# Performance work log

Measured on AMD Instinct MI355X. Metric: run time of the kernel, lower is better.

## Reference

```python
import jax, jax.numpy as jnp
import numpy as np

D_MODEL = 1024
D_HIDDEN = 32   # per-head MPS bond dimension
N_HEADS = 8
D_FF = 4096
EPS_LN = 1e-5
EPS_NORM = 1e-6


def layernorm(x, g, b):
    m = jnp.mean(x, axis=-1, keepdims=True)
    v = jnp.mean(jnp.square(x - m), axis=-1, keepdims=True)
    return (x - m) * jax.lax.rsqrt(v + EPS_LN) * g + b


def mps_recurrence(x, Wa, ba, h0, Wo, bo):
    # x: [B,S,D]. Per-token per-head transfer matrices A_t in R^{dh x dh}.
    B, S, D = x.shape
    A = (x @ Wa + ba).reshape(B, S, N_HEADS, D_HIDDEN, D_HIDDEN)
    A = jnp.moveaxis(A, 1, 0)  # [S,B,H,dh,dh]
    h_init = jnp.broadcast_to(h0, (B, N_HEADS, D_HIDDEN))  # [B,H,dh]

    def step(h, A_t):
        h = jnp.einsum('bhij,bhj->bhi', A_t, h)
        h = h / (jnp.linalg.norm(h, axis=-1, keepdims=True) + EPS_NORM)
        return h, h

    _, ys = jax.lax.scan(step, h_init, A)          # ys: [S,B,H,dh]
    ys = jnp.moveaxis(ys, 0, 1).reshape(B, S, N_HEADS * D_HIDDEN)
    return ys @ Wo + bo                            # [B,S,D]


def setup_inputs() -> dict:
    key = jax.random.key(0)
    ks = jax.random.split(key, 12)
    B, S, D = 4, 2048, D_MODEL
    inv = 1.0 / np.sqrt(D)
    inv_hd = 1.0 / np.sqrt(N_HEADS * D_HIDDEN)
    return {
        'x': jax.random.normal(ks[0], (B, S, D), jnp.float32),
        'ln1_g': jnp.ones((D,), jnp.float32),
        'ln1_b': jnp.zeros((D,), jnp.float32),
        'Wa': jax.random.normal(ks[1], (D, N_HEADS * D_HIDDEN * D_HIDDEN), jnp.float32) * inv,
        'ba': jnp.zeros((N_HEADS * D_HIDDEN * D_HIDDEN,), jnp.float32),
        'h0': jax.random.normal(ks[2], (N_HEADS, D_HIDDEN), jnp.float32) / np.sqrt(D_HIDDEN),
        'Wo': jax.random.normal(ks[3], (N_HEADS * D_HIDDEN, D), jnp.float32) * inv_hd,
        'bo': jnp.zeros((D,), jnp.float32),
        'ln2_g': jnp.ones((D,), jnp.float32),
        'ln2_b': jnp.zeros((D,), jnp.float32),
        'W1': jax.random.normal(ks[4], (D, D_FF), jnp.float32) * inv,
        'b1': jnp.zeros((D_FF,), jnp.float32),
        'W2': jax.random.normal(ks[5], (D_FF, D), jnp.float32) / np.sqrt(D_FF),
        'b2': jnp.zeros((D,), jnp.float32),
    }


def reference(x, ln1_g, ln1_b, Wa, ba, h0, Wo, bo, ln2_g, ln2_b, W1, b1, W2, b2):
    # Dropout in eval mode (identity).
    x = x + mps_recurrence(layernorm(x, ln1_g, ln1_b), Wa, ba, h0, Wo, bo)
    h = layernorm(x, ln2_g, ln2_b)
    ffn = jax.nn.gelu(h @ W1 + b1, approximate=False) @ W2 + b2
    return x + ffn
```

## Files before the change

kernel.cpp:

```cpp
#include <hip/hip_runtime.h>
#include <hip/hip_bf16.h>
#include <math.h>

typedef float f32x4 __attribute__((ext_vector_type(4)));
typedef __bf16 bf16x4 __attribute__((ext_vector_type(4)));
typedef __bf16 bf16x8 __attribute__((ext_vector_type(8)));

#define AS1(p) ((const __attribute__((address_space(1))) void*)(p))
#define AS3(p) ((__attribute__((address_space(3))) void*)(p))

static constexpr int D_MODEL = 1024;
static constexpr int S_LEN   = 2048;
static constexpr int BATCH   = 4;
static constexpr int NTOK    = BATCH * S_LEN;
static constexpr int NH      = 8;
static constexpr int DH      = 32;
static constexpr int NA      = NH * DH * DH;
static constexpr int D_FF    = 4096;
static constexpr int CHUNK   = 16;
static constexpr int NCHUNK  = S_LEN / CHUNK;

__global__ __launch_bounds__(256) void transpose_bf16(
    const float* __restrict__ in, __bf16* __restrict__ out, int R, int C) {
  __shared__ float tile[32][33];
  int tx = threadIdx.x & 31, ty = threadIdx.x >> 5;
  int c0 = blockIdx.x * 32, r0 = blockIdx.y * 32;
  for (int i = ty; i < 32; i += 8)
    tile[i][tx] = in[(size_t)(r0 + i) * C + c0 + tx];
  __syncthreads();
  for (int i = ty; i < 32; i += 8)
    out[(size_t)(c0 + i) * R + r0 + tx] = (__bf16)tile[tx][i];
}

__global__ __launch_bounds__(256) void transpose_split(
    const float* __restrict__ in, __bf16* __restrict__ ohi,
    __bf16* __restrict__ olo, int R, int C) {
  __shared__ float tile[32][33];
  int tx = threadIdx.x & 31, ty = threadIdx.x >> 5;
  int c0 = blockIdx.x * 32, r0 = blockIdx.y * 32;
  for (int i = ty; i < 32; i += 8)
    tile[i][tx] = in[(size_t)(r0 + i) * C + c0 + tx];
  __syncthreads();
  for (int i = ty; i < 32; i += 8) {
    float v = tile[tx][i];
    __bf16 h = (__bf16)v;
    ohi[(size_t)(c0 + i) * R + r0 + tx] = h;
    olo[(size_t)(c0 + i) * R + r0 + tx] = (__bf16)(v - (float)h);
  }
}

template <int MODE>
__global__ __launch_bounds__(256) void ln_kernel(
    const float* __restrict__ in, const float* __restrict__ g,
    const float* __restrict__ bta, void* __restrict__ outv,
    void* __restrict__ outv2) {
  int row = blockIdx.x, tid = threadIdx.x;
  const float4* in4 = (const float4*)(in + (size_t)row * D_MODEL);
  float4 v = in4[tid];
  float s  = v.x + v.y + v.z + v.w;
  float ss = v.x * v.x + v.y * v.y + v.z * v.z + v.w * v.w;
  for (int o = 32; o; o >>= 1) { s += __shfl_down(s, o); ss += __shfl_down(ss, o); }
  __shared__ float ps[4], pq[4];
  int lane = tid & 63, w = tid >> 6;
  if (lane == 0) { ps[w] = s; pq[w] = ss; }
  __syncthreads();
  s  = ps[0] + ps[1] + ps[2] + ps[3];
  ss = pq[0] + pq[1] + pq[2] + pq[3];
  float mean = s * (1.0f / D_MODEL);
  float var  = ss * (1.0f / D_MODEL) - mean * mean;
  float inv  = rsqrtf(fmaxf(var, 0.0f) + 1e-5f);
  float4 gv = ((const float4*)g)[tid];
  float4 bv = ((const float4*)bta)[tid];
  float o0 = (v.x - mean) * inv * gv.x + bv.x;
  float o1 = (v.y - mean) * inv * gv.y + bv.y;
  float o2 = (v.z - mean) * inv * gv.z + bv.z;
  float o3 = (v.w - mean) * inv * gv.w + bv.w;
  if (MODE == 1) {
    float4 o = {o0, o1, o2, o3};
    ((float4*)outv)[(size_t)row * (D_MODEL / 4) + tid] = o;
  } else if (MODE == 0) {
    bf16x4 o;
    o[0] = (__bf16)o0; o[1] = (__bf16)o1; o[2] = (__bf16)o2; o[3] = (__bf16)o3;
    ((bf16x4*)outv)[(size_t)row * (D_MODEL / 4) + tid] = o;
  } else {
    bf16x4 oh, ol;
    oh[0] = (__bf16)o0; oh[1] = (__bf16)o1; oh[2] = (__bf16)o2; oh[3] = (__bf16)o3;
    ol[0] = (__bf16)(o0 - (float)oh[0]);
    ol[1] = (__bf16)(o1 - (float)oh[1]);
    ol[2] = (__bf16)(o2 - (float)oh[2]);
    ol[3] = (__bf16)(o3 - (float)oh[3]);
    ((bf16x4*)outv )[(size_t)row * (D_MODEL / 4) + tid] = oh;
    ((bf16x4*)outv2)[(size_t)row * (D_MODEL / 4) + tid] = ol;
  }
}

__global__ __launch_bounds__(256) void gemm_split_f32out(
    const __bf16* __restrict__ Ahi, const __bf16* __restrict__ Alo,
    const __bf16* __restrict__ BThi, const __bf16* __restrict__ BTlo,
    const float* __restrict__ bias, float* __restrict__ out,
    int M, int N, int K) {
  __shared__ __bf16 Ash[128 * 32], Asl[128 * 32];
  __shared__ __bf16 Bsh[128 * 32], Bsl[128 * 32];
  const int tid = threadIdx.x;
  const int lane = tid & 63, w = tid >> 6;
  const int m0 = blockIdx.y * 128, n0 = blockIdx.x * 128;
  const int wm = (w >> 1) * 64, wn = (w & 1) * 64;

  f32x4 acc[4][4];
#pragma unroll
  for (int a = 0; a < 4; a++)
#pragma unroll
    for (int b = 0; b < 4; b++)
#pragma unroll
      for (int r = 0; r < 4; r++) acc[a][b][r] = 0.0f;

  const int srow = tid >> 2;
  const int soff = (tid & 3) * 16;
  const size_t goff0 = (size_t)(m0 + srow) * K + (soff >> 1);
  const size_t goff1 = (size_t)(m0 + srow + 64) * K + (soff >> 1);
  const size_t hoff0 = (size_t)(n0 + srow) * K + (soff >> 1);
  const size_t hoff1 = (size_t)(n0 + srow + 64) * K + (soff >> 1);
  const int l0 = srow * 64 + soff, l1 = (srow + 64) * 64 + soff;

  const int fm = lane & 15, fq = lane >> 4;
  for (int k0 = 0; k0 < K; k0 += 32) {
    __builtin_amdgcn_global_load_lds(AS1(Ahi + goff0 + k0), AS3((char*)Ash + l0), 16, 0, 0);
    __builtin_amdgcn_global_load_lds(AS1(Ahi + goff1 + k0), AS3((char*)Ash + l1), 16, 0, 0);
    __builtin_amdgcn_global_load_lds(AS1(Alo + goff0 + k0), AS3((char*)Asl + l0), 16, 0, 0);
    __builtin_amdgcn_global_load_lds(AS1(Alo + goff1 + k0), AS3((char*)Asl + l1), 16, 0, 0);
    __builtin_amdgcn_global_load_lds(AS1(BThi + hoff0 + k0), AS3((char*)Bsh + l0), 16, 0, 0);
    __builtin_amdgcn_global_load_lds(AS1(BThi + hoff1 + k0), AS3((char*)Bsh + l1), 16, 0, 0);
    __builtin_amdgcn_global_load_lds(AS1(BTlo + hoff0 + k0), AS3((char*)Bsl + l0), 16, 0, 0);
    __builtin_amdgcn_global_load_lds(AS1(BTlo + hoff1 + k0), AS3((char*)Bsl + l1), 16, 0, 0);
    __syncthreads();
    bf16x8 ah[4], al[4], bh[4], bl[4];
#pragma unroll
    for (int t = 0; t < 4; t++) {
      int o = (wm + t * 16 + fm) * 64 + fq * 16;
      ah[t] = *(const bf16x8*)((const char*)Ash + o);
      al[t] = *(const bf16x8*)((const char*)Asl + o);
    }
#pragma unroll
    for (int t = 0; t < 4; t++) {
      int o = (wn + t * 16 + fm) * 64 + fq * 16;
      bh[t] = *(const bf16x8*)((const char*)Bsh + o);
      bl[t] = *(const bf16x8*)((const char*)Bsl + o);
    }
#pragma unroll
    for (int tm = 0; tm < 4; tm++)
#pragma unroll
      for (int tn = 0; tn < 4; tn++) {
        acc[tm][tn] = __builtin_amdgcn_mfma_f32_16x16x32_bf16(ah[tm], bh[tn], acc[tm][tn], 0, 0, 0);
        acc[tm][tn] = __builtin_amdgcn_mfma_f32_16x16x32_bf16(ah[tm], bl[tn], acc[tm][tn], 0, 0, 0);
        acc[tm][tn] = __builtin_amdgcn_mfma_f32_16x16x32_bf16(al[tm], bh[tn], acc[tm][tn], 0, 0, 0);
      }
    __syncthreads();
  }

#pragma unroll
  for (int tn = 0; tn < 4; tn++) {
    int col = n0 + wn + tn * 16 + fm;
    float bv = bias[col];
#pragma unroll
    for (int tm = 0; tm < 4; tm++) {
#pragma unroll
      for (int r = 0; r < 4; r++) {
        int row = m0 + wm + tm * 16 + fq * 4 + r;
        out[(size_t)row * N + col] = acc[tm][tn][r] + bv;
      }
    }
  }
}

enum { EPI_BF16_BIAS = 0, EPI_BF16_BIAS_GELU = 1, EPI_F32_BIAS_RES = 2 };

template <int EPI>
__global__ __launch_bounds__(256) void gemm_bf16(
    const __bf16* __restrict__ Amat, const __bf16* __restrict__ BT,
    const float* __restrict__ bias, const float* __restrict__ res,
    void* __restrict__ out, int M, int N, int K) {
  __shared__ __bf16 As[128 * 32];
  __shared__ __bf16 Bs[128 * 32];
  const int tid = threadIdx.x;
  const int lane = tid & 63, w = tid >> 6;
  const int m0 = blockIdx.y * 128, n0 = blockIdx.x * 128;
  const int wm = (w >> 1) * 64, wn = (w & 1) * 64;

  f32x4 acc[4][4];
#pragma unroll
  for (int a = 0; a < 4; a++)
#pragma unroll
    for (int b = 0; b < 4; b++)
#pragma unroll
      for (int r = 0; r < 4; r++) acc[a][b][r] = 0.0f;

  const int srow = tid >> 2;
  const int soff = (tid & 3) * 16;
  const __bf16* gA0 = Amat + (size_t)(m0 + srow) * K + (soff >> 1);
  const __bf16* gA1 = Amat + (size_t)(m0 + srow + 64) * K + (soff >> 1);
  const __bf16* gB0 = BT + (size_t)(n0 + srow) * K + (soff >> 1);
  const __bf16* gB1 = BT + (size_t)(n0 + srow + 64) * K + (soff >> 1);
  char* lA0 = (char*)As + srow * 64 + soff;
  char* lA1 = (char*)As + (srow + 64) * 64 + soff;
  char* lB0 = (char*)Bs + srow * 64 + soff;
  char* lB1 = (char*)Bs + (srow + 64) * 64 + soff;

  const int fm = lane & 15, fq = lane >> 4;
  for (int k0 = 0; k0 < K; k0 += 32) {
    __builtin_amdgcn_global_load_lds(AS1(gA0 + k0), AS3(lA0), 16, 0, 0);
    __builtin_amdgcn_global_load_lds(AS1(gA1 + k0), AS3(lA1), 16, 0, 0);
    __builtin_amdgcn_global_load_lds(AS1(gB0 + k0), AS3(lB0), 16, 0, 0);
    __builtin_amdgcn_global_load_lds(AS1(gB1 + k0), AS3(lB1), 16, 0, 0);
    __syncthreads();
    bf16x8 af[4], bf[4];
#pragma unroll
    for (int t = 0; t < 4; t++)
      af[t] = *(const bf16x8*)((const char*)As + (wm + t * 16 + fm) * 64 + fq * 16);
#pragma unroll
    for (int t = 0; t < 4; t++)
      bf[t] = *(const bf16x8*)((const char*)Bs + (wn + t * 16 + fm) * 64 + fq * 16);
#pragma unroll
    for (int tm = 0; tm < 4; tm++)
#pragma unroll
      for (int tn = 0; tn < 4; tn++)
        acc[tm][tn] = __builtin_amdgcn_mfma_f32_16x16x32_bf16(af[tm], bf[tn], acc[tm][tn], 0, 0, 0);
    __syncthreads();
  }

#pragma unroll
  for (int tn = 0; tn < 4; tn++) {
    int col = n0 + wn + tn * 16 + fm;
    float bv = bias[col];
#pragma unroll
    for (int tm = 0; tm < 4; tm++) {
#pragma unroll
      for (int r = 0; r < 4; r++) {
        int row = m0 + wm + tm * 16 + fq * 4 + r;
        float v = acc[tm][tn][r] + bv;
        size_t idx = (size_t)row * N + col;
        if (EPI == EPI_F32_BIAS_RES) {
          ((float*)out)[idx] = v + res[idx];
        } else if (EPI == EPI_BF16_BIAS_GELU) {
          v = 0.5f * v * (1.0f + erff(v * 0.70710678118654752f));
          ((__bf16*)out)[idx] = (__bf16)v;
        } else {
          ((__bf16*)out)[idx] = (__bf16)v;
        }
      }
    }
  }
}

__global__ __launch_bounds__(64) void mps_chunkprod_f32(
    const float* __restrict__ A, float* __restrict__ P) {
  int bid = blockIdx.x;
  int c = bid & 127, hh = bid >> 7;
  int lane = threadIdx.x;
  int jj = lane & 31, half = lane >> 5;
  __shared__ float Albuf[2][DH * DH];

  float curc[32];
#pragma unroll
  for (int k = 0; k < 32; k++) curc[k] = (k == jj) ? 1.0f : 0.0f;

  const float* Abase = A + (size_t)(c * CHUNK) * NA + (size_t)hh * (DH * DH);

  {
    const float4* src = (const float4*)Abase;
    float4* dst = (float4*)Albuf[0];
#pragma unroll
    for (int r = 0; r < 4; r++) dst[lane + 64 * r] = src[lane + 64 * r];
  }
  __syncthreads();

  for (int t = 0; t < CHUNK; t++) {
    int cb = t & 1;
    float4 pf[4];
    if (t + 1 < CHUNK) {
      const float4* srcn = (const float4*)(Abase + (size_t)(t + 1) * NA);
#pragma unroll
      for (int r = 0; r < 4; r++) pf[r] = srcn[lane + 64 * r];
    }
    float nxt[16];
#pragma unroll
    for (int i16 = 0; i16 < 16; i16++) {
      const float4* ap = (const float4*)&Albuf[cb][(half * 16 + i16) * 32];
      float a0 = 0.f, a1 = 0.f, a2 = 0.f, a3 = 0.f;
#pragma unroll
      for (int k4 = 0; k4 < 8; k4++) {
        float4 av = ap[k4];
        a0 += av.x * curc[k4 * 4 + 0];
        a1 += av.y * curc[k4 * 4 + 1];
        a2 += av.z * curc[k4 * 4 + 2];
        a3 += av.w * curc[k4 * 4 + 3];
      }
      nxt[i16] = (a0 + a1) + (a2 + a3);
    }
#pragma unroll
    for (int i16 = 0; i16 < 16; i16++) {
      float mine  = nxt[i16];
      float other = __shfl_xor(mine, 32);
      curc[i16]      = (half == 0) ? mine  : other;
      curc[16 + i16] = (half == 0) ? other : mine;
    }
    if (t + 1 < CHUNK) {
      float4* dst = (float4*)Albuf[cb ^ 1];
#pragma unroll
      for (int r = 0; r < 4; r++) dst[lane + 64 * r] = pf[r];
      __syncthreads();
    }
  }

  float* Pc = P + (size_t)bid * (DH * DH);
#pragma unroll
  for (int k16 = 0; k16 < 16; k16++) {
    float v = (half == 0) ? curc[k16] : curc[16 + k16];
    Pc[(half * 16 + k16) * 32 + jj] = v;
  }
}

__global__ __launch_bounds__(64) void mps_chunkscan(
    const float* __restrict__ P, const float* __restrict__ h0,
    float* __restrict__ hstart) {
  int hh = blockIdx.x;
  int lane = threadIdx.x, i = lane & 31, half = lane >> 5;
  float hv = h0[hh * 32 + i];
  const float* row = P + (size_t)hh * NCHUNK * (DH * DH) + i * 32 + half * 16;
  int kb = half * 16;

  float4 pf0[4], pf1[4];
#pragma unroll
  for (int r = 0; r < 4; r++) pf0[r] = ((const float4*)row)[r];
#pragma unroll
  for (int r = 0; r < 4; r++) pf1[r] = ((const float4*)(row + DH * DH))[r];

  for (int c = 0; c < NCHUNK; c++) {
    if (lane < 32) hstart[((size_t)hh * NCHUNK + c) * 32 + i] = hv;
    float4 cur[4];
#pragma unroll
    for (int r = 0; r < 4; r++) cur[r] = pf0[r];
#pragma unroll
    for (int r = 0; r < 4; r++) pf0[r] = pf1[r];
    int cn = (c + 2 < NCHUNK) ? (c + 2) : (NCHUNK - 1);
#pragma unroll
    for (int r = 0; r < 4; r++)
      pf1[r] = ((const float4*)(row + (size_t)cn * (DH * DH)))[r];

    float a0 = 0.f, a1 = 0.f, a2 = 0.f, a3 = 0.f;
#pragma unroll
    for (int j4 = 0; j4 < 4; j4++) {
      float4 pv = cur[j4];
      a0 += pv.x * __shfl(hv, kb + j4 * 4 + 0);
      a1 += pv.y * __shfl(hv, kb + j4 * 4 + 1);
      a2 += pv.z * __shfl(hv, kb + j4 * 4 + 2);
      a3 += pv.w * __shfl(hv, kb + j4 * 4 + 3);
    }
    float y = (a0 + a1) + (a2 + a3);
    y += __shfl_xor(y, 32);
    float nn = y * y;
#pragma unroll
    for (int o = 16; o; o >>= 1) nn += __shfl_xor(nn, o);
    hv = y / (sqrtf(nn) + 1e-6f);
  }
}

__global__ __launch_bounds__(64) void mps_expand_f32(
    const float* __restrict__ A, const float* __restrict__ hstart,
    __bf16* __restrict__ ys, int tok0base) {
  int bid = blockIdx.x;
  int c = bid & 127, hh = bid >> 7;
  int lane = threadIdx.x, i = lane & 31, half = lane >> 5;
  float hv = hstart[(size_t)bid * 32 + i];
  const float* Ar = A + (size_t)(c * CHUNK) * NA + (size_t)hh * (DH * DH)
                    + i * 32 + half * 16;
  int kb = half * 16;

  float4 pf[4];
#pragma unroll
  for (int r = 0; r < 4; r++) pf[r] = ((const float4*)Ar)[r];

  for (int t = 0; t < CHUNK; t++) {
    float4 cur[4];
#pragma unroll
    for (int r = 0; r < 4; r++) cur[r] = pf[r];
    if (t + 1 < CHUNK) {
      const float4* an = (const float4*)(Ar + (size_t)(t + 1) * NA);
#pragma unroll
      for (int r = 0; r < 4; r++) pf[r] = an[r];
    }
    float a0 = 0.f, a1 = 0.f, a2 = 0.f, a3 = 0.f;
#pragma unroll
    for (int j4 = 0; j4 < 4; j4++) {
      float4 av = cur[j4];
      a0 += av.x * __shfl(hv, kb + j4 * 4 + 0);
      a1 += av.y * __shfl(hv, kb + j4 * 4 + 1);
      a2 += av.z * __shfl(hv, kb + j4 * 4 + 2);
      a3 += av.w * __shfl(hv, kb + j4 * 4 + 3);
    }
    float y = (a0 + a1) + (a2 + a3);
    y += __shfl_xor(y, 32);
    float nn = y * y;
#pragma unroll
    for (int o = 16; o; o >>= 1) nn += __shfl_xor(nn, o);
    hv = y / (sqrtf(nn) + 1e-6f);
    if (lane < 32)
      ys[(size_t)(tok0base + c * CHUNK + t) * (NH * DH) + hh * 32 + i] = (__bf16)hv;
  }
}

extern "C" void kernel_launch(void* const* d_in, const int* in_sizes, int n_in,
                              void* d_out, int out_size, void* d_ws, size_t ws_size,
                              hipStream_t stream) {
  const float* x     = (const float*)d_in[0];
  const float* ln1_g = (const float*)d_in[1];
  const float* ln1_b = (const float*)d_in[2];
  const float* Wa    = (const float*)d_in[3];
  const float* ba    = (const float*)d_in[4];
  const float* h0    = (const float*)d_in[5];
  const float* Wo    = (const float*)d_in[6];
  const float* bo    = (const float*)d_in[7];
  const float* ln2_g = (const float*)d_in[8];
  const float* ln2_b = (const float*)d_in[9];
  const float* W1    = (const float*)d_in[10];
  const float* b1    = (const float*)d_in[11];
  const float* W2    = (const float*)d_in[12];
  const float* b2    = (const float*)d_in[13];
  float* out = (float*)d_out;

  char* wsb = (char*)d_ws;
  size_t off = 0;
  auto alloc = [&](size_t bytes) -> void* {
    void* p = wsb + off;
    off += (bytes + 255) & ~(size_t)255;
    return p;
  };
  __bf16* WoT   = (__bf16*)alloc((size_t)(NH * DH) * D_MODEL * 2);
  __bf16* W1T   = (__bf16*)alloc((size_t)D_MODEL * D_FF * 2);
  __bf16* W2T   = (__bf16*)alloc((size_t)D_FF * D_MODEL * 2);
  __bf16* ys    = (__bf16*)alloc((size_t)NTOK * NH * DH * 2);
  float*  hst   = (float*) alloc((size_t)NH * NCHUNK * DH * 4);
  __bf16* xnh   = (__bf16*)alloc((size_t)NTOK * D_MODEL * 2);
  __bf16* xnl   = (__bf16*)alloc((size_t)NTOK * D_MODEL * 2);
  __bf16* WaTh  = (__bf16*)alloc((size_t)D_MODEL * NA * 2);
  __bf16* WaTl  = (__bf16*)alloc((size_t)D_MODEL * NA * 2);
  size_t tail0 = off;
  float*  Af32 = (float*) alloc((size_t)S_LEN * NA * 4);
  float*  P    = (float*) alloc((size_t)NH * NCHUNK * DH * DH * 4);
  __bf16* mid  = (__bf16*)(wsb + tail0);

  transpose_bf16<<<dim3(D_MODEL / 32, (NH * DH) / 32), 256, 0, stream>>>(Wo, WoT, NH * DH, D_MODEL);
  transpose_bf16<<<dim3(D_FF / 32, D_MODEL / 32), 256, 0, stream>>>(W1, W1T, D_MODEL, D_FF);
  transpose_bf16<<<dim3(D_MODEL / 32, D_FF / 32), 256, 0, stream>>>(W2, W2T, D_FF, D_MODEL);
  transpose_split<<<dim3(NA / 32, D_MODEL / 32), 256, 0, stream>>>(Wa, WaTh, WaTl, D_MODEL, NA);

  ln_kernel<2><<<NTOK, 256, 0, stream>>>(x, ln1_g, ln1_b, xnh, xnl);

  for (int b = 0; b < BATCH; b++) {
    gemm_split_f32out<<<dim3(NA / 128, S_LEN / 128), 256, 0, stream>>>(
        xnh + (size_t)b * S_LEN * D_MODEL, xnl + (size_t)b * S_LEN * D_MODEL,
        WaTh, WaTl, ba, Af32, S_LEN, NA, D_MODEL);
    mps_chunkprod_f32<<<NH * NCHUNK, 64, 0, stream>>>(Af32, P);
    mps_chunkscan<<<NH, 64, 0, stream>>>(P, h0, hst);
    mps_expand_f32<<<NH * NCHUNK, 64, 0, stream>>>(Af32, hst, ys, b * S_LEN);
  }

  gemm_bf16<EPI_F32_BIAS_RES><<<dim3(D_MODEL / 128, NTOK / 128), 256, 0, stream>>>(
      ys, WoT, bo, x, out, NTOK, D_MODEL, NH * DH);

  ln_kernel<0><<<NTOK, 256, 0, stream>>>(out, ln2_g, ln2_b, xnh, nullptr);

  gemm_bf16<EPI_BF16_BIAS_GELU><<<dim3(D_FF / 128, NTOK / 128), 256, 0, stream>>>(
      xnh, W1T, b1, nullptr, mid, NTOK, D_FF, D_MODEL);

  gemm_bf16<EPI_F32_BIAS_RES><<<dim3(D_MODEL / 128, NTOK / 128), 256, 0, stream>>>(
      mid, W2T, b2, out, out, NTOK, D_MODEL, D_FF);
}
```

Baseline: 1.571 ms.

## Swizzle GEMM blocks across XCDs, fast GELU, LDS-staged vectorized epilogue stores

Adds an XCD-aware block index remap to both GEMM kernels so that consecutive tiles share the L2 of the same die. It replaces erff in the GELU epilogue with an Abramowitz-Stegun polynomial that uses the hardware rcp and exp2 instructions. The GELU epilogue now stages its bf16 results through LDS per wave so each lane writes 16-byte rows instead of scattered 2-byte stores. The risks are slight GELU accuracy loss and the remap assuming the block count divides by 8.

```diff
diff --git a/kernel.cpp b/kernel.cpp
--- a/kernel.cpp
+++ b/kernel.cpp
@@ -19,6 +19,26 @@
 static constexpr int D_FF    = 4096;
 static constexpr int CHUNK   = 16;
 static constexpr int NCHUNK  = S_LEN / CHUNK;
+
+__device__ __forceinline__ void xcd_swizzle(int& bx, int& by) {
+  int gx = gridDim.x;
+  int nwg = gx * gridDim.y;
+  int bid = by * gx + bx;
+  int swz = (bid & 7) * (nwg >> 3) + (bid >> 3);
+  bx = swz % gx;
+  by = swz / gx;
+}
+
+__device__ __forceinline__ float gelu_erf_fast(float v) {
+  float z = fabsf(v) * 0.70710678118654752f;
+  float t = __builtin_amdgcn_rcpf(fmaf(0.3275911f, z, 1.0f));
+  float p = t * (0.254829592f + t * (-0.284496736f + t * (1.421413741f +
+            t * (-1.453152027f + t * 1.061405429f))));
+  float e = __builtin_amdgcn_exp2f(-1.4426950408889634f * z * z);
+  float er = 1.0f - p * e;
+  er = (v < 0.0f) ? -er : er;
+  return 0.5f * v * (1.0f + er);
+}
 
 __global__ __launch_bounds__(256) void transpose_bf16(
     const float* __restrict__ in, __bf16* __restrict__ out, int R, int C) {
@@ -103,7 +123,9 @@
   __shared__ __bf16 Bsh[128 * 32], Bsl[128 * 32];
   const int tid = threadIdx.x;
   const int lane = tid & 63, w = tid >> 6;
-  const int m0 = blockIdx.y * 128, n0 = blockIdx.x * 128;
+  int bx = blockIdx.x, by = blockIdx.y;
+  xcd_swizzle(bx, by);
+  const int m0 = by * 128, n0 = bx * 128;
   const int wm = (w >> 1) * 64, wn = (w & 1) * 64;
 
   f32x4 acc[4][4];
@@ -179,11 +201,14 @@
     const __bf16* __restrict__ Amat, const __bf16* __restrict__ BT,
     const float* __restrict__ bias, const float* __restrict__ res,
     void* __restrict__ out, int M, int N, int K) {
-  __shared__ __bf16 As[128 * 32];
-  __shared__ __bf16 Bs[128 * 32];
+  __shared__ __bf16 smem[2 * 128 * 32];
+  __bf16* As = smem;
+  __bf16* Bs = smem + 128 * 32;
   const int tid = threadIdx.x;
   const int lane = tid & 63, w = tid >> 6;
-  const int m0 = blockIdx.y * 128, n0 = blockIdx.x * 128;
+  int bx = blockIdx.x, by = blockIdx.y;
+  xcd_swizzle(bx, by);
+  const int m0 = by * 128, n0 = bx * 128;
   const int wm = (w >> 1) * 64, wn = (w & 1) * 64;
 
   f32x4 acc[4][4];
@@ -227,24 +252,52 @@
     __syncthreads();
   }
 
-#pragma unroll
-  for (int tn = 0; tn < 4; tn++) {
-    int col = n0 + wn + tn * 16 + fm;
-    float bv = bias[col];
-#pragma unroll
-    for (int tm = 0; tm < 4; tm++) {
-#pragma unroll
-      for (int r = 0; r < 4; r++) {
-        int row = m0 + wm + tm * 16 + fq * 4 + r;
-        float v = acc[tm][tn][r] + bv;
-        size_t idx = (size_t)row * N + col;
-        if (EPI == EPI_F32_BIAS_RES) {
-          ((float*)out)[idx] = v + res[idx];
-        } else if (EPI == EPI_BF16_BIAS_GELU) {
-          v = 0.5f * v * (1.0f + erff(v * 0.70710678118654752f));
-          ((__bf16*)out)[idx] = (__bf16)v;
-        } else {
-          ((__bf16*)out)[idx] = (__bf16)v;
+  if (EPI == EPI_BF16_BIAS_GELU) {
+    float bvs[4];
+#pragma unroll
+    for (int tn = 0; tn < 4; tn++) bvs[tn] = bias[n0 + wn + tn * 16 + fm];
+    char* patch = (char*)smem + w * 4096;
+#pragma unroll
+    for (int h2 = 0; h2 < 2; h2++) {
+#pragma unroll
+      for (int tmi = 0; tmi < 2; tmi++) {
+        int tm = h2 * 2 + tmi;
+#pragma unroll
+        for (int tn = 0; tn < 4; tn++)
+#pragma unroll
+          for (int r = 0; r < 4; r++) {
+            float vv = gelu_erf_fast(acc[tm][tn][r] + bvs[tn]);
+            *(__bf16*)(patch + (tmi * 16 + fq * 4 + r) * 128 + (tn * 16 + fm) * 2) =
+                (__bf16)vv;
+          }
+      }
+      asm volatile("s_waitcnt lgkmcnt(0)" ::: "memory");
+      int lrow = lane >> 3, lcb = (lane & 7) * 16;
+#pragma unroll
+      for (int rr = 0; rr < 4; rr++) {
+        bf16x8 ov = *(const bf16x8*)(patch + (rr * 8 + lrow) * 128 + lcb);
+        size_t grow = (size_t)(m0 + wm + h2 * 32 + rr * 8 + lrow);
+        *(bf16x8*)((__bf16*)out + grow * N + n0 + wn + (lane & 7) * 8) = ov;
+      }
+      if (h2 == 0) asm volatile("s_waitcnt lgkmcnt(0)" ::: "memory");
+    }
+  } else {
+#pragma unroll
+    for (int tn = 0; tn < 4; tn++) {
+      int col = n0 + wn + tn * 16 + fm;
+      float bv = bias[col];
+#pragma unroll
+      for (int tm = 0; tm < 4; tm++) {
+#pragma unroll
+        for (int r = 0; r < 4; r++) {
+          int row = m0 + wm + tm * 16 + fq * 4 + r;
+          float v = acc[tm][tn][r] + bv;
+          size_t idx = (size_t)row * N + col;
+          if (EPI == EPI_F32_BIAS_RES) {
+            ((float*)out)[idx] = v + res[idx];
+          } else {
+            ((__bf16*)out)[idx] = (__bf16)v;
+          }
         }
       }
     }
```

New measurement: 1.565 ms. Within noise of the previous version (-0.3%).
